# Kernel optimization log

Measured on AMD Instinct MI355X. Metric: run time of the kernel, lower is better.

## Reference

```python
import jax, jax.numpy as jnp
import numpy as np

N_NODES = 50000
N_EDGES = 800000
D_IN = 128
D_HID = 128
D_EMB = 128
D_OUT = 2


def _mean_aggr(feat, src, dst, n_nodes):
    # gather source-node features along edges, segment-mean at destinations
    msg = feat[src]                                               # [E, d]
    s = jax.ops.segment_sum(msg, dst, num_segments=n_nodes)      # [N, d]
    cnt = jax.ops.segment_sum(jnp.ones((src.shape[0], 1), feat.dtype), dst,
                              num_segments=n_nodes)               # [N, 1]
    return s / jnp.maximum(cnt, 1.0)


def _sage_conv(h, src, dst, W_l, W_r, b, n_nodes):
    # PyG SAGEConv: lin_l(mean_j h_j) + lin_r(h_i);  W_* are [out, in]
    agg = _mean_aggr(h, src, dst, n_nodes)
    return agg @ W_l.T + h @ W_r.T + b


def setup_inputs() -> dict:
    key = jax.random.key(0)
    ks = jax.random.split(key, 12)

    def w(k, out_d, in_d):
        return jax.random.normal(k, (out_d, in_d), jnp.float32) * (1.0 / np.sqrt(in_d))

    x = jax.random.normal(ks[0], (N_NODES, D_IN), jnp.float32)
    edge_index = jax.random.randint(ks[1], (2, N_EDGES), 0, N_NODES, dtype=jnp.int64)
    return {
        "x": x,
        "edge_index": edge_index,
        "Wl1": w(ks[2], D_HID, D_IN), "Wr1": w(ks[3], D_HID, D_IN),
        "b1": jnp.zeros((D_HID,), jnp.float32),
        "Wl2": w(ks[4], D_HID, D_HID), "Wr2": w(ks[5], D_HID, D_HID),
        "b2": jnp.zeros((D_HID,), jnp.float32),
        "Wl3": w(ks[6], D_EMB, D_HID), "Wr3": w(ks[7], D_EMB, D_HID),
        "b3": jnp.zeros((D_EMB,), jnp.float32),
        "Wo": w(ks[8], D_OUT, D_EMB),
        "bo": jnp.zeros((D_OUT,), jnp.float32),
    }


def reference(x, edge_index, Wl1, Wr1, b1, Wl2, Wr2, b2, Wl3, Wr3, b3, Wo, bo):
    src, dst = edge_index[0], edge_index[1]
    n = x.shape[0]
    h = jax.nn.relu(_sage_conv(x, src, dst, Wl1, Wr1, b1, n))   # sage1 + relu (dropout=0)
    h = jax.nn.relu(_sage_conv(h, src, dst, Wl2, Wr2, b2, n))   # hidden sage + relu
    h = _sage_conv(h, src, dst, Wl3, Wr3, b3, n)                # sage2 (no relu)
    out = h @ Wo.T + bo                                          # decoder linear
    return (out, h)
```

## Files before the change

### kernel.cpp

```cpp
#include <hip/hip_runtime.h>


#define N_NODES 50000
#define N_EDGES 800000
#define D 128
#define NB ((N_NODES + 255) / 256)

typedef __bf16 bf16x8 __attribute__((ext_vector_type(8)));
typedef float f32x4 __attribute__((ext_vector_type(4)));

struct bf16pair { bf16x8 hi, lo; };

__device__ inline bf16pair split8(const float* __restrict__ p) {
    f32x4 a = *reinterpret_cast<const f32x4*>(p);
    f32x4 b = *reinterpret_cast<const f32x4*>(p + 4);
    bf16pair r;
#pragma unroll
    for (int i = 0; i < 4; ++i) {
        float v = a[i];
        __bf16 h = (__bf16)v;
        r.hi[i] = h;
        r.lo[i] = (__bf16)(v - (float)h);
    }
#pragma unroll
    for (int i = 0; i < 4; ++i) {
        float v = b[i];
        __bf16 h = (__bf16)v;
        r.hi[4 + i] = h;
        r.lo[4 + i] = (__bf16)(v - (float)h);
    }
    return r;
}

__global__ void detect_kernel(const int* __restrict__ ew, int* __restrict__ flag) {
    __shared__ int s;
    if (threadIdx.x == 0) s = 0;
    __syncthreads();
    int v = 0;
    for (int i = threadIdx.x; i < 1024; i += 256) v |= ew[2 * i + 1];
    if (v) atomicOr(&s, 1);
    __syncthreads();
    if (threadIdx.x == 0) flag[0] = s ? 1 : 2;
}

__global__ void count_kernel(const int* __restrict__ ew, const int* __restrict__ flag,
                             int* __restrict__ cnt) {
    int st = flag[0];
    int e = blockIdx.x * blockDim.x + threadIdx.x;
    if (e < N_EDGES) {
        int d = ew[(size_t)st * (N_EDGES + e)];
        atomicAdd(&cnt[d], 1);
    }
}

__global__ __launch_bounds__(256) void scan1_kernel(const int* __restrict__ cnt,
                                                    int* __restrict__ off,
                                                    int* __restrict__ bsum) {
    const int tid = threadIdx.x, lane = tid & 63, wid = tid >> 6;
    const int i = blockIdx.x * 256 + tid;
    int orig = (i < N_NODES) ? cnt[i] : 0;
    int v = orig;
#pragma unroll
    for (int d = 1; d < 64; d <<= 1) {
        int t = __shfl_up(v, d, 64);
        if (lane >= d) v += t;
    }
    __shared__ int ws[4];
    if (lane == 63) ws[wid] = v;
    __syncthreads();
    int base = 0;
    for (int w = 0; w < wid; ++w) base += ws[w];
    v += base;
    if (i < N_NODES) off[i] = v - orig;
    if (tid == 255) bsum[blockIdx.x] = v;
}

__global__ __launch_bounds__(256) void scan2_kernel(const int* __restrict__ bsum,
                                                    int* __restrict__ bbase,
                                                    int* __restrict__ off) {
    const int tid = threadIdx.x, lane = tid & 63, wid = tid >> 6;
    int orig = (tid < NB) ? bsum[tid] : 0;
    int v = orig;
#pragma unroll
    for (int d = 1; d < 64; d <<= 1) {
        int t = __shfl_up(v, d, 64);
        if (lane >= d) v += t;
    }
    __shared__ int ws[4];
    if (lane == 63) ws[wid] = v;
    __syncthreads();
    int base = 0;
    for (int w = 0; w < wid; ++w) base += ws[w];
    v += base;
    if (tid < NB) bbase[tid] = v - orig;
    if (tid == NB - 1) off[N_NODES] = v;
}

__global__ __launch_bounds__(256) void scan3_kernel(int* __restrict__ off,
                                                    const int* __restrict__ bbase,
                                                    int* __restrict__ cursor) {
    int i = blockIdx.x * 256 + threadIdx.x;
    if (i < N_NODES) {
        int v = off[i] + bbase[blockIdx.x];
        off[i] = v;
        cursor[i] = v;
    }
}

__global__ void fill_kernel(const int* __restrict__ ew, const int* __restrict__ flag,
                            int* __restrict__ cursor, int* __restrict__ csr) {
    int st = flag[0];
    int e = blockIdx.x * blockDim.x + threadIdx.x;
    if (e < N_EDGES) {
        int d = ew[(size_t)st * (N_EDGES + e)];
        int sidx = ew[(size_t)st * e];
        int pos = atomicAdd(&cursor[d], 1);
        csr[pos] = sidx;
    }
}

__global__ __launch_bounds__(256) void aggregate_kernel(const float* __restrict__ h,
                                                        const int* __restrict__ off,
                                                        const int* __restrict__ csr,
                                                        float* __restrict__ agg) {
    int gw = blockIdx.x * 4 + (threadIdx.x >> 6);
    int lane = threadIdx.x & 63;
    if (gw >= N_NODES) return;
    int beg = off[gw], end = off[gw + 1];
    float ax = 0.f, ay = 0.f;
    int j = beg;
    for (; j + 3 < end; j += 4) {
        int s0 = csr[j], s1 = csr[j + 1], s2 = csr[j + 2], s3 = csr[j + 3];
        float2 v0 = *reinterpret_cast<const float2*>(h + (size_t)s0 * D + lane * 2);
        float2 v1 = *reinterpret_cast<const float2*>(h + (size_t)s1 * D + lane * 2);
        float2 v2 = *reinterpret_cast<const float2*>(h + (size_t)s2 * D + lane * 2);
        float2 v3 = *reinterpret_cast<const float2*>(h + (size_t)s3 * D + lane * 2);
        ax += v0.x + v1.x + v2.x + v3.x;
        ay += v0.y + v1.y + v2.y + v3.y;
    }
    for (; j < end; ++j) {
        int s = csr[j];
        float2 v = *reinterpret_cast<const float2*>(h + (size_t)s * D + lane * 2);
        ax += v.x;
        ay += v.y;
    }
    int c = end - beg;
    if (c < 1) c = 1;
    float fc = (float)c;
    float2 o;
    o.x = ax / fc;
    o.y = ay / fc;
    *reinterpret_cast<float2*>(agg + (size_t)gw * D + lane * 2) = o;
}

__global__ __launch_bounds__(256) void gemm_kernel(const float* __restrict__ A1,
                                                   const float* __restrict__ A2,
                                                   const float* __restrict__ W1,
                                                   const float* __restrict__ W2,
                                                   const float* __restrict__ bias,
                                                   float* __restrict__ out,
                                                   int do_relu) {
    const int lane = threadIdx.x & 63;
    const int wid = threadIdx.x >> 6;
    const int colbase = wid * 32;
    const int lr = lane & 15;
    const int lg = lane >> 4;

    bf16pair B1[2][4], B2[2][4];
    for (int ct = 0; ct < 2; ++ct) {
        int j = colbase + ct * 16 + lr;
        for (int kk = 0; kk < 4; ++kk) {
            int k = kk * 32 + lg * 8;
            B1[ct][kk] = split8(W1 + j * D + k);
            B2[ct][kk] = split8(W2 + j * D + k);
        }
    }
    float bb0 = bias[colbase + lr];
    float bb1 = bias[colbase + 16 + lr];

    const int ntiles = N_NODES / 16;
    for (int rt = blockIdx.x; rt < ntiles; rt += gridDim.x) {
        int row = rt * 16 + lr;
        bf16pair Af1[4], Af2[4];
        for (int kk = 0; kk < 4; ++kk) {
            int k = kk * 32 + lg * 8;
            Af1[kk] = split8(A1 + (size_t)row * D + k);
            Af2[kk] = split8(A2 + (size_t)row * D + k);
        }
        for (int ct = 0; ct < 2; ++ct) {
            float bb = ct ? bb1 : bb0;
            f32x4 acc = {bb, bb, bb, bb};
            for (int kk = 0; kk < 4; ++kk) {
                acc = __builtin_amdgcn_mfma_f32_16x16x32_bf16(Af1[kk].hi, B1[ct][kk].hi, acc, 0, 0, 0);
                acc = __builtin_amdgcn_mfma_f32_16x16x32_bf16(Af1[kk].lo, B1[ct][kk].hi, acc, 0, 0, 0);
                acc = __builtin_amdgcn_mfma_f32_16x16x32_bf16(Af1[kk].hi, B1[ct][kk].lo, acc, 0, 0, 0);
                acc = __builtin_amdgcn_mfma_f32_16x16x32_bf16(Af2[kk].hi, B2[ct][kk].hi, acc, 0, 0, 0);
                acc = __builtin_amdgcn_mfma_f32_16x16x32_bf16(Af2[kk].lo, B2[ct][kk].hi, acc, 0, 0, 0);
                acc = __builtin_amdgcn_mfma_f32_16x16x32_bf16(Af2[kk].hi, B2[ct][kk].lo, acc, 0, 0, 0);
            }
            int col = colbase + ct * 16 + lr;
            for (int r = 0; r < 4; ++r) {
                float v = acc[r];
                if (do_relu) v = fmaxf(v, 0.0f);
                int orow = rt * 16 + lg * 4 + r;
                out[(size_t)orow * D + col] = v;
            }
        }
    }
}

__global__ __launch_bounds__(256) void decoder_kernel(const float* __restrict__ h,
                                                      const float* __restrict__ Wo,
                                                      const float* __restrict__ bo,
                                                      float* __restrict__ out) {
    int lane = threadIdx.x & 63;
    int wid = blockIdx.x * 4 + (threadIdx.x >> 6);
    int nw = gridDim.x * 4;
    float2 w0 = *reinterpret_cast<const float2*>(Wo + lane * 2);
    float2 w1 = *reinterpret_cast<const float2*>(Wo + D + lane * 2);
    float b0 = bo[0], b1 = bo[1];
    for (int i = wid; i < N_NODES; i += nw) {
        float2 v = *reinterpret_cast<const float2*>(h + (size_t)i * D + lane * 2);
        float d0 = v.x * w0.x + v.y * w0.y;
        float d1 = v.x * w1.x + v.y * w1.y;
        for (int m = 1; m < 64; m <<= 1) {
            d0 += __shfl_xor(d0, m, 64);
            d1 += __shfl_xor(d1, m, 64);
        }
        if (lane == 0) {
            float2 o;
            o.x = d0 + b0;
            o.y = d1 + b1;
            *reinterpret_cast<float2*>(out + (size_t)i * 2) = o;
        }
    }
}

extern "C" void kernel_launch(void* const* d_in, const int* in_sizes, int n_in,
                              void* d_out, int out_size, void* d_ws, size_t ws_size,
                              hipStream_t stream) {
    const float* x   = (const float*)d_in[0];
    const int* ew    = (const int*)d_in[1];
    const float* Wl1 = (const float*)d_in[2];
    const float* Wr1 = (const float*)d_in[3];
    const float* b1  = (const float*)d_in[4];
    const float* Wl2 = (const float*)d_in[5];
    const float* Wr2 = (const float*)d_in[6];
    const float* b2  = (const float*)d_in[7];
    const float* Wl3 = (const float*)d_in[8];
    const float* Wr3 = (const float*)d_in[9];
    const float* b3  = (const float*)d_in[10];
    const float* Wo  = (const float*)d_in[11];
    const float* bo  = (const float*)d_in[12];

    char* ws = (char*)d_ws;
    size_t o = 0;
    auto alloc = [&](size_t bytes) {
        char* p = ws + o;
        o += (bytes + 255) & ~(size_t)255;
        return p;
    };
    int* flag   = (int*)alloc(4);
    int* cnt    = (int*)alloc((size_t)N_NODES * 4);
    int* off    = (int*)alloc((size_t)(N_NODES + 1) * 4);
    int* cursor = (int*)alloc((size_t)N_NODES * 4);
    int* csr    = (int*)alloc((size_t)N_EDGES * 4);
    int* bsum   = (int*)alloc((size_t)NB * 4);
    int* bbase  = (int*)alloc((size_t)NB * 4);
    float* agg  = (float*)alloc((size_t)N_NODES * D * 4);
    float* h1   = (float*)alloc((size_t)N_NODES * D * 4);
    float* h2   = (float*)alloc((size_t)N_NODES * D * 4);

    float* outp = (float*)d_out;
    float* h3   = outp + (size_t)N_NODES * 2;

    hipMemsetAsync(cnt, 0, (size_t)N_NODES * 4, stream);
    detect_kernel<<<1, 256, 0, stream>>>(ew, flag);
    count_kernel<<<(N_EDGES + 255) / 256, 256, 0, stream>>>(ew, flag, cnt);
    scan1_kernel<<<NB, 256, 0, stream>>>(cnt, off, bsum);
    scan2_kernel<<<1, 256, 0, stream>>>(bsum, bbase, off);
    scan3_kernel<<<NB, 256, 0, stream>>>(off, bbase, cursor);
    fill_kernel<<<(N_EDGES + 255) / 256, 256, 0, stream>>>(ew, flag, cursor, csr);

    const int AGG_BLOCKS = (N_NODES + 3) / 4;

    aggregate_kernel<<<AGG_BLOCKS, 256, 0, stream>>>(x, off, csr, agg);
    gemm_kernel<<<512, 256, 0, stream>>>(agg, x, Wl1, Wr1, b1, h1, 1);

    aggregate_kernel<<<AGG_BLOCKS, 256, 0, stream>>>(h1, off, csr, agg);
    gemm_kernel<<<512, 256, 0, stream>>>(agg, h1, Wl2, Wr2, b2, h2, 1);

    aggregate_kernel<<<AGG_BLOCKS, 256, 0, stream>>>(h2, off, csr, agg);
    gemm_kernel<<<512, 256, 0, stream>>>(agg, h2, Wl3, Wr3, b3, h3, 0);

    decoder_kernel<<<2048, 256, 0, stream>>>(h3, Wo, bo, outp);
}
```

Measured before the change: 479.0 us.

## Fuse neighbor aggregation, SAGE GEMM and decoder into one per-layer kernel

Each layer now runs one kernel that gathers and mean-aggregates neighbor features for a 16-row tile into swizzled shared memory, then feeds them straight into the split-bf16 MFMA GEMM. This removes the agg buffer round trip through global memory and several launches. The last layer also computes the 2-wide decoder output in its epilogue using shuffles and a shared reduction, so the separate decoder pass disappears. The fill kernel's CSR store becomes nontemporal. In exchange, the gather latency now sits in the GEMM kernel with only 512 blocks and extra barriers, which can reduce the memory parallelism available to the irregular gather.

```diff
diff --git a/kernel.cpp b/kernel.cpp
--- a/kernel.cpp
+++ b/kernel.cpp
@@ -5,15 +5,14 @@
 #define N_EDGES 800000
 #define D 128
 #define NB ((N_NODES + 255) / 256)
+#define NTILES (N_NODES / 16)
 
 typedef __bf16 bf16x8 __attribute__((ext_vector_type(8)));
 typedef float f32x4 __attribute__((ext_vector_type(4)));
 
 struct bf16pair { bf16x8 hi, lo; };
 
-__device__ inline bf16pair split8(const float* __restrict__ p) {
-    f32x4 a = *reinterpret_cast<const f32x4*>(p);
-    f32x4 b = *reinterpret_cast<const f32x4*>(p + 4);
+__device__ inline bf16pair split8v(f32x4 a, f32x4 b) {
     bf16pair r;
 #pragma unroll
     for (int i = 0; i < 4; ++i) {
@@ -30,6 +29,11 @@
         r.lo[4 + i] = (__bf16)(v - (float)h);
     }
     return r;
+}
+
+__device__ inline bf16pair split8(const float* __restrict__ p) {
+    return split8v(*reinterpret_cast<const f32x4*>(p),
+                   *reinterpret_cast<const f32x4*>(p + 4));
 }
 
 __global__ void detect_kernel(const int* __restrict__ ew, int* __restrict__ flag) {
@@ -115,51 +119,23 @@
         int d = ew[(size_t)st * (N_EDGES + e)];
         int sidx = ew[(size_t)st * e];
         int pos = atomicAdd(&cursor[d], 1);
-        csr[pos] = sidx;
-    }
-}
-
-__global__ __launch_bounds__(256) void aggregate_kernel(const float* __restrict__ h,
-                                                        const int* __restrict__ off,
-                                                        const int* __restrict__ csr,
-                                                        float* __restrict__ agg) {
-    int gw = blockIdx.x * 4 + (threadIdx.x >> 6);
-    int lane = threadIdx.x & 63;
-    if (gw >= N_NODES) return;
-    int beg = off[gw], end = off[gw + 1];
-    float ax = 0.f, ay = 0.f;
-    int j = beg;
-    for (; j + 3 < end; j += 4) {
-        int s0 = csr[j], s1 = csr[j + 1], s2 = csr[j + 2], s3 = csr[j + 3];
-        float2 v0 = *reinterpret_cast<const float2*>(h + (size_t)s0 * D + lane * 2);
-        float2 v1 = *reinterpret_cast<const float2*>(h + (size_t)s1 * D + lane * 2);
-        float2 v2 = *reinterpret_cast<const float2*>(h + (size_t)s2 * D + lane * 2);
-        float2 v3 = *reinterpret_cast<const float2*>(h + (size_t)s3 * D + lane * 2);
-        ax += v0.x + v1.x + v2.x + v3.x;
-        ay += v0.y + v1.y + v2.y + v3.y;
-    }
-    for (; j < end; ++j) {
-        int s = csr[j];
-        float2 v = *reinterpret_cast<const float2*>(h + (size_t)s * D + lane * 2);
-        ax += v.x;
-        ay += v.y;
-    }
-    int c = end - beg;
-    if (c < 1) c = 1;
-    float fc = (float)c;
-    float2 o;
-    o.x = ax / fc;
-    o.y = ay / fc;
-    *reinterpret_cast<float2*>(agg + (size_t)gw * D + lane * 2) = o;
-}
-
-__global__ __launch_bounds__(256) void gemm_kernel(const float* __restrict__ A1,
-                                                   const float* __restrict__ A2,
-                                                   const float* __restrict__ W1,
-                                                   const float* __restrict__ W2,
-                                                   const float* __restrict__ bias,
-                                                   float* __restrict__ out,
-                                                   int do_relu) {
+        __builtin_nontemporal_store(sidx, &csr[pos]);
+    }
+}
+
+__global__ __launch_bounds__(256) void fused_kernel(const float* __restrict__ hin,
+                                                    const int* __restrict__ off,
+                                                    const int* __restrict__ csr,
+                                                    const float* __restrict__ W1,
+                                                    const float* __restrict__ W2,
+                                                    const float* __restrict__ bias,
+                                                    float* __restrict__ hout,
+                                                    int do_relu,
+                                                    const float* __restrict__ Wo,
+                                                    const float* __restrict__ bo,
+                                                    float* __restrict__ dec) {
+    __shared__ float sAgg[16 * 128];
+    __shared__ float part[4][16][2];
     const int lane = threadIdx.x & 63;
     const int wid = threadIdx.x >> 6;
     const int colbase = wid * 32;
@@ -177,16 +153,61 @@
     }
     float bb0 = bias[colbase + lr];
     float bb1 = bias[colbase + 16 + lr];
-
-    const int ntiles = N_NODES / 16;
-    for (int rt = blockIdx.x; rt < ntiles; rt += gridDim.x) {
-        int row = rt * 16 + lr;
+    const int decode = (dec != nullptr);
+    float wo00 = 0.f, wo01 = 0.f, wo10 = 0.f, wo11 = 0.f, bo0 = 0.f, bo1 = 0.f;
+    if (decode) {
+        wo00 = Wo[colbase + lr];       wo01 = Wo[colbase + 16 + lr];
+        wo10 = Wo[D + colbase + lr];   wo11 = Wo[D + colbase + 16 + lr];
+        bo0 = bo[0];                   bo1 = bo[1];
+    }
+
+    for (int rt = blockIdx.x; rt < NTILES; rt += gridDim.x) {
+        __syncthreads();
+        for (int rr = 0; rr < 4; ++rr) {
+            int row = wid * 4 + rr;
+            int node = rt * 16 + row;
+            int beg = off[node], end = off[node + 1];
+            float ax = 0.f, ay = 0.f;
+            int j = beg;
+            for (; j + 7 < end; j += 8) {
+                int s0 = csr[j],     s1 = csr[j + 1], s2 = csr[j + 2], s3 = csr[j + 3];
+                int s4 = csr[j + 4], s5 = csr[j + 5], s6 = csr[j + 6], s7 = csr[j + 7];
+                float2 v0 = *reinterpret_cast<const float2*>(hin + (size_t)s0 * D + lane * 2);
+                float2 v1 = *reinterpret_cast<const float2*>(hin + (size_t)s1 * D + lane * 2);
+                float2 v2 = *reinterpret_cast<const float2*>(hin + (size_t)s2 * D + lane * 2);
+                float2 v3 = *reinterpret_cast<const float2*>(hin + (size_t)s3 * D + lane * 2);
+                float2 v4 = *reinterpret_cast<const float2*>(hin + (size_t)s4 * D + lane * 2);
+                float2 v5 = *reinterpret_cast<const float2*>(hin + (size_t)s5 * D + lane * 2);
+                float2 v6 = *reinterpret_cast<const float2*>(hin + (size_t)s6 * D + lane * 2);
+                float2 v7 = *reinterpret_cast<const float2*>(hin + (size_t)s7 * D + lane * 2);
+                ax += (v0.x + v1.x) + (v2.x + v3.x) + (v4.x + v5.x) + (v6.x + v7.x);
+                ay += (v0.y + v1.y) + (v2.y + v3.y) + (v4.y + v5.y) + (v6.y + v7.y);
+            }
+            for (; j < end; ++j) {
+                int s = csr[j];
+                float2 v = *reinterpret_cast<const float2*>(hin + (size_t)s * D + lane * 2);
+                ax += v.x;
+                ay += v.y;
+            }
+            int c = end - beg;
+            if (c < 1) c = 1;
+            float fc = (float)c;
+            int unit = ((lane >> 2) + row) & 15;
+            int phys = row * 128 + unit * 8 + (lane & 3) * 2;
+            sAgg[phys] = ax / fc;
+            sAgg[phys + 1] = ay / fc;
+        }
+        __syncthreads();
         bf16pair Af1[4], Af2[4];
         for (int kk = 0; kk < 4; ++kk) {
             int k = kk * 32 + lg * 8;
-            Af1[kk] = split8(A1 + (size_t)row * D + k);
-            Af2[kk] = split8(A2 + (size_t)row * D + k);
-        }
+            int unit = ((k >> 3) + lr) & 15;
+            const float* ap = &sAgg[lr * 128 + unit * 8];
+            Af1[kk] = split8v(*reinterpret_cast<const f32x4*>(ap),
+                              *reinterpret_cast<const f32x4*>(ap + 4));
+            Af2[kk] = split8(hin + (size_t)(rt * 16 + lr) * D + k);
+        }
+        float p0[4] = {0.f, 0.f, 0.f, 0.f}, p1[4] = {0.f, 0.f, 0.f, 0.f};
         for (int ct = 0; ct < 2; ++ct) {
             float bb = ct ? bb1 : bb0;
             f32x4 acc = {bb, bb, bb, bb};
@@ -198,40 +219,43 @@
                 acc = __builtin_amdgcn_mfma_f32_16x16x32_bf16(Af2[kk].lo, B2[ct][kk].hi, acc, 0, 0, 0);
                 acc = __builtin_amdgcn_mfma_f32_16x16x32_bf16(Af2[kk].hi, B2[ct][kk].lo, acc, 0, 0, 0);
             }
+            float woa = ct ? wo01 : wo00;
+            float wob = ct ? wo11 : wo10;
             int col = colbase + ct * 16 + lr;
             for (int r = 0; r < 4; ++r) {
                 float v = acc[r];
                 if (do_relu) v = fmaxf(v, 0.0f);
                 int orow = rt * 16 + lg * 4 + r;
-                out[(size_t)orow * D + col] = v;
-            }
-        }
-    }
-}
-
-__global__ __launch_bounds__(256) void decoder_kernel(const float* __restrict__ h,
-                                                      const float* __restrict__ Wo,
-                                                      const float* __restrict__ bo,
-                                                      float* __restrict__ out) {
-    int lane = threadIdx.x & 63;
-    int wid = blockIdx.x * 4 + (threadIdx.x >> 6);
-    int nw = gridDim.x * 4;
-    float2 w0 = *reinterpret_cast<const float2*>(Wo + lane * 2);
-    float2 w1 = *reinterpret_cast<const float2*>(Wo + D + lane * 2);
-    float b0 = bo[0], b1 = bo[1];
-    for (int i = wid; i < N_NODES; i += nw) {
-        float2 v = *reinterpret_cast<const float2*>(h + (size_t)i * D + lane * 2);
-        float d0 = v.x * w0.x + v.y * w0.y;
-        float d1 = v.x * w1.x + v.y * w1.y;
-        for (int m = 1; m < 64; m <<= 1) {
-            d0 += __shfl_xor(d0, m, 64);
-            d1 += __shfl_xor(d1, m, 64);
-        }
-        if (lane == 0) {
-            float2 o;
-            o.x = d0 + b0;
-            o.y = d1 + b1;
-            *reinterpret_cast<float2*>(out + (size_t)i * 2) = o;
+                hout[(size_t)orow * D + col] = v;
+                p0[r] += v * woa;
+                p1[r] += v * wob;
+            }
+        }
+        if (decode) {
+#pragma unroll
+            for (int m = 1; m < 16; m <<= 1) {
+#pragma unroll
+                for (int r = 0; r < 4; ++r) {
+                    p0[r] += __shfl_xor(p0[r], m, 64);
+                    p1[r] += __shfl_xor(p1[r], m, 64);
+                }
+            }
+            if (lr == 0) {
+#pragma unroll
+                for (int r = 0; r < 4; ++r) {
+                    part[wid][lg * 4 + r][0] = p0[r];
+                    part[wid][lg * 4 + r][1] = p1[r];
+                }
+            }
+            __syncthreads();
+            if (wid == 0 && lane < 16) {
+                float s0 = part[0][lane][0] + part[1][lane][0] + part[2][lane][0] + part[3][lane][0] + bo0;
+                float s1 = part[0][lane][1] + part[1][lane][1] + part[2][lane][1] + part[3][lane][1] + bo1;
+                float2 o;
+                o.x = s0;
+                o.y = s1;
+                *reinterpret_cast<float2*>(dec + (size_t)(rt * 16 + lane) * 2) = o;
+            }
         }
     }
 }
@@ -267,7 +291,6 @@
     int* csr    = (int*)alloc((size_t)N_EDGES * 4);
     int* bsum   = (int*)alloc((size_t)NB * 4);
     int* bbase  = (int*)alloc((size_t)NB * 4);
-    float* agg  = (float*)alloc((size_t)N_NODES * D * 4);
     float* h1   = (float*)alloc((size_t)N_NODES * D * 4);
     float* h2   = (float*)alloc((size_t)N_NODES * D * 4);
 
@@ -282,16 +305,10 @@
     scan3_kernel<<<NB, 256, 0, stream>>>(off, bbase, cursor);
     fill_kernel<<<(N_EDGES + 255) / 256, 256, 0, stream>>>(ew, flag, cursor, csr);
 
-    const int AGG_BLOCKS = (N_NODES + 3) / 4;
-
-    aggregate_kernel<<<AGG_BLOCKS, 256, 0, stream>>>(x, off, csr, agg);
-    gemm_kernel<<<512, 256, 0, stream>>>(agg, x, Wl1, Wr1, b1, h1, 1);
-
-    aggregate_kernel<<<AGG_BLOCKS, 256, 0, stream>>>(h1, off, csr, agg);
-    gemm_kernel<<<512, 256, 0, stream>>>(agg, h1, Wl2, Wr2, b2, h2, 1);
-
-    aggregate_kernel<<<AGG_BLOCKS, 256, 0, stream>>>(h2, off, csr, agg);
-    gemm_kernel<<<512, 256, 0, stream>>>(agg, h2, Wl3, Wr3, b3, h3, 0);
-
-    decoder_kernel<<<2048, 256, 0, stream>>>(h3, Wo, bo, outp);
-}
+    fused_kernel<<<512, 256, 0, stream>>>(x, off, csr, Wl1, Wr1, b1, h1, 1,
+                                          nullptr, nullptr, nullptr);
+    fused_kernel<<<512, 256, 0, stream>>>(h1, off, csr, Wl2, Wr2, b2, h2, 1,
+                                          nullptr, nullptr, nullptr);
+    fused_kernel<<<512, 256, 0, stream>>>(h2, off, csr, Wl3, Wr3, b3, h3, 0,
+                                          Wo, bo, outp);
+}
```

New measurement: 618.7 us. +29.2%, slower.
